# Kernel optimization log

Hardware: AMD Instinct MI355X
Metric: run time of the kernel (lower is better)

The kernel has to match this reference:

```python
import jax, jax.numpy as jnp
import numpy as np

VOCAB = 128000
SEED = 42
BATCH = 256
SEQ = 128
BIAS_FACTOR = 2.0
TOP_P = 0.9


def setup_inputs() -> dict:
    key = jax.random.key(0)
    k1, k2 = jax.random.split(key)
    input_ids = jax.random.randint(k1, (BATCH, SEQ), 0, VOCAB, dtype=jnp.int64 if jax.config.jax_enable_x64 else jnp.int32)
    scores = jax.random.normal(k2, (BATCH, VOCAB), dtype=jnp.float32) * 4.0
    # green list generated exactly as in the torch module: numpy rng, 0/1 per vocab entry
    green = jnp.asarray(np.random.default_rng(SEED).integers(0, 2, VOCAB), dtype=jnp.float32)
    return {"input_ids": input_ids, "scores": scores, "green": green}


def reference(input_ids, scores, green):
    B, V = scores.shape
    # bias green tokens, softmax over vocab
    logits = scores + BIAS_FACTOR * green[None, :]          # [B, V]
    probs = jax.nn.softmax(logits, axis=-1)                 # [B, V]
    # descending sort (torch.sort(descending=True))
    sorted_idx = jnp.argsort(-probs, axis=-1)               # [B, V]
    sorted_probs = jnp.take_along_axis(probs, sorted_idx, axis=-1)
    cum = jnp.cumsum(sorted_probs, axis=-1)                 # [B, V]
    # torch.searchsorted(cum, top_p, right=False): first i with cum[i] >= top_p
    cutoff = jnp.sum(cum < TOP_P, axis=-1, keepdims=True)   # [B, 1]
    # keep positions 0..cutoff inclusive (original zeroes cutoff+1:)
    keep = jnp.arange(V)[None, :] <= cutoff                 # [B, V]
    kept = jnp.where(keep, sorted_probs, 0.0)
    kept = kept / jnp.sum(kept, axis=-1, keepdims=True)
    kept = jnp.where(jnp.isfinite(kept), kept, 0.0)
    # multinomial(1) over truncated renormalized probs
    samp = jax.random.categorical(jax.random.key(1), jnp.log(kept), axis=-1)  # [B]
    next_tok = jnp.take_along_axis(sorted_idx, samp[:, None], axis=-1)[:, 0]  # [B]
    # scores[b,:] = 1e-5; scores[b, next_token] = 1e5
    out = jnp.full((B, V), 1e-5, dtype=scores.dtype)
    out = out.at[jnp.arange(B), next_tok].set(1e5)
    return out
```

## Files before the change

### kernel.cpp

```cpp
#include <hip/hip_runtime.h>
#include <cstdint>
#include <cstddef>

#define BATCH 256
#define VOCAB 128000
#define V4 (VOCAB/4)
#define NBINS 4096
#define CAP 4096
#define WSEG 256
#define NSEG 32
#define SPILLCAP 6144
#define GATE_SPILL 8.0f
#define SPILL_BIN 3088u
#define GATE_HIST 1.0f
#define M44 0xFFFFFFFFFFFull
#define FIX 16777216.0f
#define FIXINV 5.9604644775390625e-8f

__device__ __forceinline__ uint32_t rotl32(uint32_t v, int r){ return (v<<r)|(v>>(32-r)); }

__device__ __forceinline__ void threefry2x32_01(uint32_t& x0, uint32_t& x1){
  const uint32_t ks0=0u, ks1=1u, ks2=0x1BD11BDAu ^ 0u ^ 1u;
  x0+=ks0; x1+=ks1;
#define TF_R(r) { x0+=x1; x1=rotl32(x1,(r)); x1^=x0; }
  TF_R(13) TF_R(15) TF_R(26) TF_R(6)
  x0+=ks1; x1+=ks2+1u;
  TF_R(17) TF_R(29) TF_R(16) TF_R(24)
  x0+=ks2; x1+=ks0+2u;
  TF_R(13) TF_R(15) TF_R(26) TF_R(6)
  x0+=ks0; x1+=ks1+3u;
  TF_R(17) TF_R(29) TF_R(16) TF_R(24)
  x0+=ks1; x1+=ks2+4u;
  TF_R(13) TF_R(15) TF_R(26) TF_R(6)
  x0+=ks2; x1+=ks0+5u;
#undef TF_R
}

__device__ __forceinline__ float gumbel_at(uint32_t z){
  uint32_t x0 = 0u, x1 = z;
  threefry2x32_01(x0, x1);
  uint32_t bits = x0 ^ x1;
  uint32_t fb = (bits >> 9) | 0x3F800000u;
  float f = __uint_as_float(fb) - 1.0f;
  const float tiny = 1.17549435e-38f;
  float uu = fmaxf(tiny, f + tiny);
  return -logf(-logf(uu));
}

__device__ __forceinline__ uint32_t fkey(uint32_t u){
  return (u >> 31) ? ~u : (u | 0x80000000u);
}
__device__ __forceinline__ float pdecode(unsigned long long k){
  return __uint_as_float(~(uint32_t)(k >> 32));
}

__global__ __launch_bounds__(256, 4) void k_stream(
    const float* __restrict__ scores, const float* __restrict__ green,
    float* __restrict__ out, unsigned long long* __restrict__ spill,
    unsigned* __restrict__ counts, float* __restrict__ pmax,
    float* __restrict__ psum)
{
  const int blk = blockIdx.x;
  const int b = blk >> 3, q = blk & 7;
  const int tid = threadIdx.x, lane = tid & 63, wv = tid >> 6;
  const int base = q * 4000;
  const float4* row4 = (const float4*)(scores + (size_t)b * VOCAB);
  const float4* grn4 = (const float4*)green;
  float4* o4 = (float4*)(out + (size_t)b * VOCAB);
  const int sidx = (q << 2) | wv;
  unsigned long long* seg = spill + ((size_t)b * NSEG + sidx) * WSEG;
  const float4 fv = make_float4(1e-5f, 1e-5f, 1e-5f, 1e-5f);

  float lm = -INFINITY, ls16 = 0.f;
  unsigned wcnt = 0u;

#define SP1(LV, IDX) do { \
    float l_ = (LV); \
    lm = fmaxf(lm, l_); \
    ls16 += expf(l_ - 16.0f); \
    bool pr_ = (l_ >= GATE_SPILL); \
    unsigned long long mk_ = __ballot(pr_); \
    if (pr_){ \
      unsigned pos_ = wcnt + (unsigned)__popcll(mk_ & ((1ull << lane) - 1ull)); \
      if (pos_ < WSEG) \
        seg[pos_] = ((unsigned long long)__float_as_uint(l_) << 32) | (IDX); \
    } \
    wcnt += (unsigned)__popcll(mk_); \
  } while(0)

#define SP4(SV, GV, II) do { \
    SP1(fmaf(2.f, (GV).x, (SV).x), (unsigned)(4*(II)+0)); \
    SP1(fmaf(2.f, (GV).y, (SV).y), (unsigned)(4*(II)+1)); \
    SP1(fmaf(2.f, (GV).z, (SV).z), (unsigned)(4*(II)+2)); \
    SP1(fmaf(2.f, (GV).w, (SV).w), (unsigned)(4*(II)+3)); \
  } while(0)

  float4 sa, sb, sc, sd, ga, gb, gc, gd;
  {
    const int i0 = base + tid;
    sa = row4[i0]; sb = row4[i0+256]; sc = row4[i0+512]; sd = row4[i0+768];
    ga = grn4[i0]; gb = grn4[i0+256]; gc = grn4[i0+512]; gd = grn4[i0+768];
  }
  #pragma unroll
  for (int g = 0; g < 3; ++g){
    const int cur = base + tid + g*1024;
    const int nxt = cur + 1024;
    float4 ta, tb, tc, td, ua, ub, uc, ud;
    if (g < 2){
      ta = row4[nxt]; tb = row4[nxt+256]; tc = row4[nxt+512]; td = row4[nxt+768];
      ua = grn4[nxt]; ub = grn4[nxt+256]; uc = grn4[nxt+512]; ud = grn4[nxt+768];
    } else {
      ta = row4[nxt]; tb = row4[nxt+256]; tc = row4[nxt+512];
      ua = grn4[nxt]; ub = grn4[nxt+256]; uc = grn4[nxt+512];
      td = tc; ud = uc;
    }
    o4[cur] = fv; o4[cur+256] = fv; o4[cur+512] = fv; o4[cur+768] = fv;
    SP4(sa, ga, cur); SP4(sb, gb, cur+256); SP4(sc, gc, cur+512); SP4(sd, gd, cur+768);
    sa = ta; sb = tb; sc = tc; sd = td; ga = ua; gb = ub; gc = uc; gd = ud;
  }
  {
    const int i0 = base + 3072 + tid;
    o4[i0] = fv; o4[i0+256] = fv; o4[i0+512] = fv;
    SP4(sa, ga, i0); SP4(sb, gb, i0+256); SP4(sc, gc, i0+512);
  }
  if (tid < 160){
    const int i0 = base + 3840 + tid;
    float4 s = row4[i0];
    float4 g = grn4[i0];
    o4[i0] = fv;
    SP4(s, g, i0);
  }
#undef SP4
#undef SP1

  for (int off = 32; off > 0; off >>= 1){
    lm = fmaxf(lm, __shfl_down(lm, off, 64));
    ls16 += __shfl_down(ls16, off, 64);
  }
  if (lane == 0){
    const int gi = b * NSEG + sidx;
    pmax[gi] = lm; psum[gi] = ls16; counts[gi] = wcnt;
  }
}

__global__ __launch_bounds__(1024) void k_row(
    const float* __restrict__ scores, const float* __restrict__ green,
    float* __restrict__ out, const unsigned long long* __restrict__ spill,
    const unsigned* __restrict__ counts, const float* __restrict__ pmax,
    const float* __restrict__ psum)
{
  __shared__ unsigned long long sp64[SPILLCAP];
  __shared__ union {
    unsigned long long hist[NBINS];
    unsigned long long skeys[CAP];
  } u;
  __shared__ float red[1024];
  __shared__ unsigned long long wavewin[16];
  __shared__ unsigned segoff[NSEG + 1];
  __shared__ float m_sh, s16_sh;
  __shared__ unsigned n_sh, thr_sh, fb_sh;
  __shared__ int cut_sh;

  const int b = blockIdx.x, tid = threadIdx.x;
  const float* srow = scores + (size_t)b * VOCAB;
  float* orow = out + (size_t)b * VOCAB;

  for (int i = tid; i < NBINS; i += 1024) u.hist[i] = 0ull;
  if (tid == 0){
    unsigned tot = 0u, fb = 0u;
    float mm = -INFINITY, ss = 0.f;
    for (int s = 0; s < NSEG; ++s){
      unsigned c = counts[b*NSEG + s];
      segoff[s] = tot;
      if (c > WSEG) fb = 1u;
      tot += c;
      mm = fmaxf(mm, pmax[b*NSEG + s]);
      ss += psum[b*NSEG + s];
    }
    segoff[NSEG] = tot;
    if (tot > SPILLCAP) fb = 1u;
    m_sh = mm; s16_sh = ss; fb_sh = fb; n_sh = 0u;
  }
  __syncthreads();
  const float m = m_sh, S16 = s16_sh;
  const unsigned tot = segoff[NSEG];
  unsigned fb = fb_sh;

  if (!fb){
    for (int s = 0; s < NSEG; ++s){
      const unsigned c0 = segoff[s], cl = segoff[s+1] - c0;
      const unsigned long long* seg = spill + ((size_t)b*NSEG + s)*WSEG;
      for (unsigned j = tid; j < cl; j += 1024) sp64[c0 + j] = seg[j];
    }
    __syncthreads();
    for (unsigned j = tid; j < tot; j += 1024){
      uint32_t lb = (uint32_t)(sp64[j] >> 32);
      atomicAdd(&u.hist[fkey(lb) >> 20],
                (1ull<<44) | (unsigned long long)(expf(__uint_as_float(lb) - 16.0f) * FIX));
    }
    __syncthreads();
    if (tid == 0){
      float target = 0.903f * S16;
      int top = (int)(fkey(__float_as_uint(m)) >> 20);
      float acc = 0.f; unsigned c = 0; unsigned result = (unsigned)top;
      for (int bin = top; bin >= 0; --bin){
        unsigned long long h = u.hist[bin];
        unsigned cb = (unsigned)(h >> 44);
        if (c + cb > CAP) break;
        acc += (float)(h & M44) * FIXINV; c += cb; result = (unsigned)bin;
        if (acc >= target) break;
      }
      thr_sh = result;
      if (result < SPILL_BIN) fb_sh = 1u;
    }
    __syncthreads();
    fb = fb_sh;
  }

  if (fb){
    for (int i = tid; i < NBINS; i += 1024) u.hist[i] = 0ull;
    __syncthreads();
    const float4* row4 = (const float4*)srow;
    const float4* grn4 = (const float4*)green;
    for (int i = tid; i < V4; i += 1024){
      float4 s = row4[i], g = grn4[i];
      #pragma unroll
      for (int c = 0; c < 4; ++c){
        float l = fmaf(2.f, (&g.x)[c], (&s.x)[c]);
        if (l >= GATE_HIST)
          atomicAdd(&u.hist[fkey(__float_as_uint(l)) >> 20],
                    (1ull<<44) | (unsigned long long)(expf(l - 16.0f) * FIX));
      }
    }
    __syncthreads();
    if (tid == 0){
      float target = 0.903f * S16;
      int top = (int)(fkey(__float_as_uint(m)) >> 20);
      float acc = 0.f; unsigned c = 0; unsigned result = (unsigned)top;
      for (int bin = top; bin >= 0; --bin){
        unsigned long long h = u.hist[bin];
        unsigned cb = (unsigned)(h >> 44);
        if (c + cb > CAP) break;
        acc += (float)(h & M44) * FIXINV; c += cb; result = (unsigned)bin;
        if (acc >= target) break;
      }
      thr_sh = result;
    }
    __syncthreads();
    const unsigned thr = thr_sh;
    for (int i = tid; i < V4; i += 1024){
      float4 s = row4[i], g = grn4[i];
      #pragma unroll
      for (int c = 0; c < 4; ++c){
        float l = fmaf(2.f, (&g.x)[c], (&s.x)[c]);
        if ((fkey(__float_as_uint(l)) >> 20) >= thr){
          unsigned pos = atomicAdd(&n_sh, 1u);
          float p = expf(l - 16.0f) / S16;
          if (pos < CAP)
            u.skeys[pos] = ((unsigned long long)(~__float_as_uint(p)) << 32) | (unsigned)(4*i + c);
        }
      }
    }
  } else {
    const unsigned thr = thr_sh;
    for (unsigned j = tid; j < tot; j += 1024){
      unsigned long long k = sp64[j];
      uint32_t lb = (uint32_t)(k >> 32);
      if ((fkey(lb) >> 20) >= thr){
        unsigned pos = atomicAdd(&n_sh, 1u);
        float p = expf(__uint_as_float(lb) - 16.0f) / S16;
        if (pos < CAP)
          u.skeys[pos] = ((unsigned long long)(~__float_as_uint(p)) << 32) | (k & 0xFFFFFFFFull);
      }
    }
  }
  __syncthreads();
  unsigned n = n_sh; if (n > CAP) n = CAP;

  unsigned N2 = 2; while (N2 < n) N2 <<= 1;
  for (unsigned i = n + tid; i < N2; i += 1024) u.skeys[i] = 0xFFFFFFFFFFFFFFFFull;
  __syncthreads();
  for (unsigned k = 2; k <= N2; k <<= 1){
    for (unsigned j = k >> 1; j > 0; j >>= 1){
      for (unsigned i = tid; i < N2; i += 1024){
        unsigned ixj = i ^ j;
        if (ixj > i){
          unsigned long long a = u.skeys[i], c2 = u.skeys[ixj];
          bool up = ((i & k) == 0u);
          if ((a > c2) == up){ u.skeys[i] = c2; u.skeys[ixj] = a; }
        }
      }
      __syncthreads();
    }
  }

  unsigned C = (n + 1023) >> 10;
  {
    unsigned lo = tid * C; if (lo > n) lo = n;
    unsigned hi = lo + C;  if (hi > n) hi = n;
    float s = 0.f;
    for (unsigned j = lo; j < hi; ++j) s += pdecode(u.skeys[j]);
    red[tid] = s;
  }
  __syncthreads();
  if (tid == 0){
    float run = 0.f; int cut = (int)n - 1; int t = 0;
    for (; t < 1024; ++t){ float cs = red[t]; if (run + cs >= 0.9f) break; run += cs; }
    if (t < 1024){
      float c2 = run;
      for (unsigned j = (unsigned)t * C; j < n; ++j){
        c2 += pdecode(u.skeys[j]);
        if (c2 >= 0.9f){ cut = (int)j; break; }
      }
    }
    cut_sh = cut;
  }
  __syncthreads();
  const int cut = cut_sh;

  float best = -INFINITY; unsigned bj = 0x7FFFFFFFu;
  for (int j = tid; j <= cut; j += 1024){
    float p = pdecode(u.skeys[j]);
    float sc = logf(p) + gumbel_at((uint32_t)b * (uint32_t)VOCAB + (uint32_t)j);
    if (sc > best || (sc == best && (unsigned)j < bj)){ best = sc; bj = (unsigned)j; }
  }
  for (int off = 32; off > 0; off >>= 1){
    float osc = __shfl_down(best, off, 64);
    unsigned oj = __shfl_down(bj, off, 64);
    if (osc > best || (osc == best && oj < bj)){ best = osc; bj = oj; }
  }
  if ((tid & 63) == 0){
    uint32_t ub = __float_as_uint(best);
    uint32_t ou = (ub >> 31) ? ~ub : (ub | 0x80000000u);
    wavewin[tid >> 6] = ((unsigned long long)ou << 32) |
                        (unsigned long long)(0xFFFFFFFFu - bj);
  }
  __syncthreads();
  if (tid == 0){
    unsigned long long bb = 0ull;
    for (int w = 0; w < 16; ++w){ unsigned long long x = wavewin[w]; if (x > bb) bb = x; }
    unsigned jwin = 0xFFFFFFFFu - (unsigned)(bb & 0xFFFFFFFFull);
    orow[(size_t)(u.skeys[jwin] & 0xFFFFFFFFull)] = 1e5f;
  }
}

extern "C" void kernel_launch(void* const* d_in, const int* in_sizes, int n_in,
                              void* d_out, int out_size, void* d_ws, size_t ws_size,
                              hipStream_t stream) {
  const float* scores = (const float*)d_in[1];
  const float* green  = (const float*)d_in[2];
  float* out = (float*)d_out;

  unsigned long long* spill = (unsigned long long*)d_ws;
  unsigned* counts = (unsigned*)(spill + (size_t)BATCH * NSEG * WSEG);
  float* pmax = (float*)(counts + BATCH * NSEG);
  float* psum = pmax + BATCH * NSEG;
  (void)ws_size;

  hipLaunchKernelGGL(k_stream, dim3(BATCH*8), dim3(256),  0, stream,
                     scores, green, out, spill, counts, pmax, psum);
  hipLaunchKernelGGL(k_row,    dim3(BATCH),   dim3(1024), 0, stream,
                     scores, green, out, spill, counts, pmax, psum);
}
```

Before: 332.4 us.

## Parallelize row-kernel serial steps and use nontemporal fill stores

Writes the 1e-5 fill of the output with nontemporal stores so it does not pollute cache. In the row kernel, segment metadata is loaded into shared memory in parallel, and spill segments are gathered with one flat loop instead of a per-segment loop. The fallback compaction uses wave-level ballot so there is one atomic per wave. The serial single-thread cutoff scan is replaced by a parallel Hillis-Steele prefix sum over per-thread partial sums. The prefix sum adds about 20 barriers and changes float summation order, which may shift the cutoff slightly compared with the serial scan.

```diff
diff --git a/kernel.cpp b/kernel.cpp
--- a/kernel.cpp
+++ b/kernel.cpp
@@ -52,6 +52,12 @@
 }
 __device__ __forceinline__ float pdecode(unsigned long long k){
   return __uint_as_float(~(uint32_t)(k >> 32));
+}
+
+typedef float vfloat4 __attribute__((ext_vector_type(4)));
+__device__ __forceinline__ void ntstore4(float4* p, float4 v){
+  vfloat4 nv; nv.x = v.x; nv.y = v.y; nv.z = v.z; nv.w = v.w;
+  __builtin_nontemporal_store(nv, (vfloat4*)p);
 }
 
 __global__ __launch_bounds__(256, 4) void k_stream(
@@ -114,20 +120,21 @@
       ua = grn4[nxt]; ub = grn4[nxt+256]; uc = grn4[nxt+512];
       td = tc; ud = uc;
     }
-    o4[cur] = fv; o4[cur+256] = fv; o4[cur+512] = fv; o4[cur+768] = fv;
+    ntstore4(&o4[cur], fv); ntstore4(&o4[cur+256], fv);
+    ntstore4(&o4[cur+512], fv); ntstore4(&o4[cur+768], fv);
     SP4(sa, ga, cur); SP4(sb, gb, cur+256); SP4(sc, gc, cur+512); SP4(sd, gd, cur+768);
     sa = ta; sb = tb; sc = tc; sd = td; ga = ua; gb = ub; gc = uc; gd = ud;
   }
   {
     const int i0 = base + 3072 + tid;
-    o4[i0] = fv; o4[i0+256] = fv; o4[i0+512] = fv;
+    ntstore4(&o4[i0], fv); ntstore4(&o4[i0+256], fv); ntstore4(&o4[i0+512], fv);
     SP4(sa, ga, i0); SP4(sb, gb, i0+256); SP4(sc, gc, i0+512);
   }
   if (tid < 160){
     const int i0 = base + 3840 + tid;
     float4 s = row4[i0];
     float4 g = grn4[i0];
-    o4[i0] = fv;
+    ntstore4(&o4[i0], fv);
     SP4(s, g, i0);
   }
 #undef SP4
@@ -156,26 +163,33 @@
   } u;
   __shared__ float red[1024];
   __shared__ unsigned long long wavewin[16];
-  __shared__ unsigned segoff[NSEG + 1];
+  __shared__ unsigned segcnt[NSEG], segoff[NSEG + 1];
+  __shared__ float pm_sh[NSEG], ps_sh[NSEG];
   __shared__ float m_sh, s16_sh;
   __shared__ unsigned n_sh, thr_sh, fb_sh;
   __shared__ int cut_sh;
 
-  const int b = blockIdx.x, tid = threadIdx.x;
+  const int b = blockIdx.x, tid = threadIdx.x, lane = tid & 63;
   const float* srow = scores + (size_t)b * VOCAB;
   float* orow = out + (size_t)b * VOCAB;
 
+  if (tid < NSEG){
+    segcnt[tid] = counts[b*NSEG + tid];
+    pm_sh[tid]  = pmax[b*NSEG + tid];
+    ps_sh[tid]  = psum[b*NSEG + tid];
+  }
   for (int i = tid; i < NBINS; i += 1024) u.hist[i] = 0ull;
+  __syncthreads();
   if (tid == 0){
     unsigned tot = 0u, fb = 0u;
     float mm = -INFINITY, ss = 0.f;
     for (int s = 0; s < NSEG; ++s){
-      unsigned c = counts[b*NSEG + s];
+      unsigned c = segcnt[s];
       segoff[s] = tot;
       if (c > WSEG) fb = 1u;
       tot += c;
-      mm = fmaxf(mm, pmax[b*NSEG + s]);
-      ss += psum[b*NSEG + s];
+      mm = fmaxf(mm, pm_sh[s]);
+      ss += ps_sh[s];
     }
     segoff[NSEG] = tot;
     if (tot > SPILLCAP) fb = 1u;
@@ -187,10 +201,10 @@
   unsigned fb = fb_sh;
 
   if (!fb){
-    for (int s = 0; s < NSEG; ++s){
-      const unsigned c0 = segoff[s], cl = segoff[s+1] - c0;
-      const unsigned long long* seg = spill + ((size_t)b*NSEG + s)*WSEG;
-      for (unsigned j = tid; j < cl; j += 1024) sp64[c0 + j] = seg[j];
+    const unsigned long long* segbase = spill + (size_t)b * NSEG * WSEG;
+    for (int slot = tid; slot < NSEG*WSEG; slot += 1024){
+      const int s = slot >> 8, j = slot & (WSEG-1);
+      if ((unsigned)j < segcnt[s]) sp64[segoff[s] + j] = segbase[slot];
     }
     __syncthreads();
     for (unsigned j = tid; j < tot; j += 1024){
@@ -263,11 +277,20 @@
     }
   } else {
     const unsigned thr = thr_sh;
-    for (unsigned j = tid; j < tot; j += 1024){
-      unsigned long long k = sp64[j];
-      uint32_t lb = (uint32_t)(k >> 32);
-      if ((fkey(lb) >> 20) >= thr){
-        unsigned pos = atomicAdd(&n_sh, 1u);
+    const unsigned iters = (tot + 1023) >> 10;
+    for (unsigned it = 0; it < iters; ++it){
+      const unsigned j = it*1024 + tid;
+      bool pass = false; unsigned long long k = 0ull; uint32_t lb = 0u;
+      if (j < tot){
+        k = sp64[j]; lb = (uint32_t)(k >> 32);
+        pass = (fkey(lb) >> 20) >= thr;
+      }
+      unsigned long long mk = __ballot(pass);
+      unsigned wbase = 0u;
+      if (lane == 0) wbase = atomicAdd(&n_sh, (unsigned)__popcll(mk));
+      wbase = (unsigned)__shfl((int)wbase, 0, 64);
+      if (pass){
+        unsigned pos = wbase + (unsigned)__popcll(mk & ((1ull << lane) - 1ull));
         float p = expf(__uint_as_float(lb) - 16.0f) / S16;
         if (pos < CAP)
           u.skeys[pos] = ((unsigned long long)(~__float_as_uint(p)) << 32) | (k & 0xFFFFFFFFull);
@@ -294,7 +317,7 @@
     }
   }
 
-  unsigned C = (n + 1023) >> 10;
+  const unsigned C = (n + 1023) >> 10;
   {
     unsigned lo = tid * C; if (lo > n) lo = n;
     unsigned hi = lo + C;  if (hi > n) hi = n;
@@ -302,18 +325,27 @@
     for (unsigned j = lo; j < hi; ++j) s += pdecode(u.skeys[j]);
     red[tid] = s;
   }
-  __syncthreads();
-  if (tid == 0){
-    float run = 0.f; int cut = (int)n - 1; int t = 0;
-    for (; t < 1024; ++t){ float cs = red[t]; if (run + cs >= 0.9f) break; run += cs; }
-    if (t < 1024){
-      float c2 = run;
-      for (unsigned j = (unsigned)t * C; j < n; ++j){
+  if (tid == 0) cut_sh = (int)n - 1;
+  __syncthreads();
+  for (int off = 1; off < 1024; off <<= 1){
+    float v = red[tid];
+    float w = (tid >= off) ? red[tid - off] : 0.f;
+    __syncthreads();
+    red[tid] = v + w;
+    __syncthreads();
+  }
+  {
+    float incl = red[tid];
+    float excl = (tid == 0) ? 0.f : red[tid - 1];
+    if (excl < 0.9f && incl >= 0.9f){
+      float c2 = excl;
+      unsigned lo = tid * C; if (lo > n) lo = n;
+      unsigned hi = lo + C;  if (hi > n) hi = n;
+      for (unsigned j = lo; j < hi; ++j){
         c2 += pdecode(u.skeys[j]);
-        if (c2 >= 0.9f){ cut = (int)j; break; }
-      }
-    }
-    cut_sh = cut;
+        if (c2 >= 0.9f){ cut_sh = (int)j; break; }
+      }
+    }
   }
   __syncthreads();
   const int cut = cut_sh;
```

Measured after the change: 302.1 us. 1.1x faster.
